# Kernel tuning notes

Hardware: AMD Instinct MI355X
Metric: run time of the kernel (lower is better)

The kernel has to match this reference:

```python
import jax, jax.numpy as jnp
import numpy as np

XY = 16   # xy_size
Z = 16    # z_size
S = XY * XY * Z   # num_states = 4096
V = 2048  # num_tokens


def _build_structure():
    # Static 3D-grid neighbor structure (replaces the per-state Python loop).
    h = np.arange(S)
    zc, rem = np.divmod(h, XY * XY)
    yc, xc = np.divmod(rem, XY)
    coords = np.stack([xc, yc, zc], 1)                       # [S,3] (x,y,z)
    offs = np.array([[0, 0, 0], [1, 0, 0], [-1, 0, 0], [0, 1, 0],
                     [0, -1, 0], [0, 0, 1], [0, 0, 2]])       # 7 fixed offsets
    nc = coords[:, None, :] + offs[None]                      # [S,7,3]
    valid = ((nc[..., 0] >= 0) & (nc[..., 0] < XY) &
             (nc[..., 1] >= 0) & (nc[..., 1] < XY) &
             (nc[..., 2] >= 0) & (nc[..., 2] < Z))
    dest = nc[..., 0] + XY * (nc[..., 1] + XY * nc[..., 2])   # flat neighbor idx
    # compact valid neighbors to the front, preserving offset order:
    # j-th valid neighbor consumes logit j (matches logits[h, :len(valid)])
    order = np.argsort(~valid, axis=1, kind='stable')
    tgt = np.take_along_axis(dest, order, axis=1)
    vmask = np.take_along_axis(valid, order, axis=1)
    tgt = np.where(vmask, tgt, S)  # invalid slots -> dummy column S
    return jnp.asarray(tgt), jnp.asarray(vmask)

TGT, VMASK = _build_structure()


def transition_log_p(trans_w):
    # masked log-softmax over the first k valid logits of each row
    logits = jnp.where(VMASK, trans_w, -1e30)
    logp = jax.nn.log_softmax(logits, axis=1)
    logp = jnp.where(VMASK, logp, -jnp.inf)
    T = jnp.full((S, S + 1), -jnp.inf, trans_w.dtype)
    T = T.at[jnp.arange(S)[:, None], TGT].set(logp)
    return T[:, :S]  # [S,S], row h = log p(transition targets of h)


def smoothed_emission(emis_w):
    em = jax.nn.log_softmax(emis_w, axis=-1).reshape(Z, XY, XY, V)
    lv, rv = em[:, :, :1], em[:, :, -1:]
    lh, rh = em[:, :1], em[:, -1:]
    c = jnp.zeros((Z, 1, 1, V), em.dtype)  # log(1)=0 pad, as in the original
    c2 = lambda *a: jnp.concatenate(a, axis=2)
    c1 = lambda *a: jnp.concatenate(a, axis=1)
    up = c1(c2(lv, em, rv), c2(c, rh, c), c2(c, rh, c))
    dn = c1(c2(c, lh, c), c2(c, lh, c), c2(lv, em, rv))
    lf = c1(c2(lh, c, c), c2(em, rv, rv), c2(rh, c, c))
    rt = c1(c2(c, c, lh), c2(lv, lv, em), c2(c, c, rh))
    cr = c1(c2(c, lh, c), c2(lv, em, rv), c2(c, rh, c))
    mean = jax.nn.logsumexp(jnp.stack((up, dn, lf, rt, cr)), axis=0) - jnp.log(5.0)
    return mean[:, 1:-1, 1:-1].reshape(S, V)


def _forward(stories, trans_w, emis_w, prior_w):
    priors = jax.nn.log_softmax(prior_w)                      # [S]
    em = smoothed_emission(emis_w)                            # [S,V]
    padded = jnp.concatenate([em, jnp.zeros((S, 1), em.dtype)], axis=1)  # [S,V+1]
    # per-(story, step) emission log-prob: sum over sentence tokens
    all_emis = padded.T[stories].sum(axis=2)                  # [B,L,S]
    all_emis = jnp.transpose(all_emis, (1, 0, 2))             # [L,B,S]
    T = transition_log_p(trans_w)                             # [S,S]
    amax = jnp.max(T, axis=1, keepdims=True)                  # [S,1], finite (self-loop)
    P = jnp.exp(T - amax)                                     # [S,S]
    score0 = all_emis[0] + priors                             # [B,S]

    def step(score, em_t):
        # new[b,a] = em_t[b,a] + logsumexp_h(T[a,h] + score[b,h])  (stable log-matmul)
        smax = jnp.max(score, axis=1, keepdims=True)          # [B,1]
        new = em_t + jnp.log(jnp.exp(score - smax) @ P.T) + smax + amax.T
        return new, new

    _, rest = jax.lax.scan(step, score0, all_emis[1:])
    return jnp.concatenate([score0[None], rest], axis=0)      # [L,B,S]


def setup_inputs() -> dict:
    key = jax.random.key(0)
    k1, k2, k3, k4 = jax.random.split(key, 4)
    B, L, W = 8, 32, 8
    return {
        "stories_tensor": jax.random.randint(k1, (B, L, W), 0, V + 1, dtype=jnp.int32),
        "story_length": L,
        "trans_w": jax.random.normal(k2, (S, 7), jnp.float32),
        "emis_w": jax.random.normal(k3, (S, V), jnp.float32),
        "prior_w": jax.random.normal(k4, (S,), jnp.float32),
    }


def reference(stories_tensor, story_length, trans_w, emis_w, prior_w):
    assert stories_tensor.shape[1] == story_length
    return _forward(stories_tensor, trans_w, emis_w, prior_w)
```

## Files before the change

kernel.cpp:

```cpp
#include <hip/hip_runtime.h>
#include <math.h>

#define XYD 16
#define ZD 16
#define SS 4096
#define VV 2048
#define BB 8
#define LL 32
#define WW 8
#define VC 32
#define SM_STRIDE 257

#define GUARD_L 16
#define GUARD_R 512
#define EBUF_N (GUARD_L + SS + GUARD_R)

#define BAR() asm volatile("s_waitcnt lgkmcnt(0)\n\ts_barrier" ::: "memory")

typedef unsigned short us8 __attribute__((ext_vector_type(8)));

__device__ __forceinline__ float b2f(unsigned short u) {
    union { unsigned int i; float f; } x; x.i = ((unsigned int)u) << 16; return x.f;
}
__device__ __forceinline__ unsigned short f2b(float f) {
    union { float f; unsigned int i; } x; x.f = f; return (unsigned short)(x.i >> 16);
}

__global__ void k_logZ(const float* __restrict__ emis_w, float* __restrict__ logZ) {
    int wave = threadIdx.x >> 6;
    int lane = threadIdx.x & 63;
    int row  = blockIdx.x * 4 + wave;
    const float* r = emis_w + (size_t)row * VV;
    float vals[32];
    float m = -INFINITY;
#pragma unroll
    for (int k = 0; k < 8; k++) {
        float4 f = ((const float4*)r)[k * 64 + lane];
        vals[k*4+0] = f.x; vals[k*4+1] = f.y; vals[k*4+2] = f.z; vals[k*4+3] = f.w;
    }
#pragma unroll
    for (int k = 0; k < 32; k++) m = fmaxf(m, vals[k]);
#pragma unroll
    for (int o = 32; o; o >>= 1) m = fmaxf(m, __shfl_xor(m, o));
    float sum = 0.f;
#pragma unroll
    for (int k = 0; k < 32; k++) sum += __expf(vals[k] - m);
#pragma unroll
    for (int o = 32; o; o >>= 1) sum += __shfl_xor(sum, o);
    if (lane == 0) logZ[row] = m + __logf(sum);
}

__global__ void k_smooth(const float* __restrict__ emis_w, const float* __restrict__ logZ,
                         unsigned short* __restrict__ smTb) {
    __shared__ float tileT[VC * SM_STRIDE];
    int z  = blockIdx.x;
    int v0 = blockIdx.y * VC;
    int tid = threadIdx.x;
    int rsub = tid >> 3;
    int c0   = (tid & 7) * 4;

#pragma unroll
    for (int it = 0; it < 8; it++) {
        int r  = it * 32 + rsub;
        int sg = z * 256 + r;
        float lz = logZ[sg];
        float4 w = *(const float4*)(emis_w + (size_t)sg * VV + v0 + c0);
        tileT[(c0+0)*SM_STRIDE + r] = __expf(w.x - lz);
        tileT[(c0+1)*SM_STRIDE + r] = __expf(w.y - lz);
        tileT[(c0+2)*SM_STRIDE + r] = __expf(w.z - lz);
        tileT[(c0+3)*SM_STRIDE + r] = __expf(w.w - lz);
    }
    __syncthreads();

    int x = tid & 15, y = tid >> 4;
    int sxp = (x < 15) ? tid + 1  : tid;
    int sxm = (x > 0)  ? tid - 1  : tid;
    int syp = (y < 15) ? tid + 16 : tid;
    int sym = (y > 0)  ? tid - 16 : tid;
    unsigned short* o = smTb + (size_t)v0 * SS + z * 256 + tid;
#pragma unroll
    for (int i = 0; i < VC; i++) {
        const float* tb = tileT + i * SM_STRIDE;
        float s = tb[tid] + tb[sxp] + tb[sxm] + tb[syp] + tb[sym];
        o[(size_t)i * SS] = f2b(__logf(s * 0.2f));
    }
}

__global__ void __launch_bounds__(512) k_emis(
    const int* __restrict__ stories, const unsigned short* __restrict__ smTb,
    float* __restrict__ all_emis) {
    int blk = blockIdx.x;
    int t = blk >> 3, b = blk & 7;
    int tid = threadIdx.x;
    int tok[WW];
#pragma unroll
    for (int w = 0; w < WW; w++) tok[w] = stories[(b * LL + t) * WW + w];
    int s0 = tid * 8;
    float acc[8] = {0.f,0.f,0.f,0.f,0.f,0.f,0.f,0.f};
#pragma unroll
    for (int w = 0; w < WW; w++) {
        if (tok[w] < VV) {
            us8 u = *(const us8*)(smTb + (size_t)tok[w] * SS + s0);
#pragma unroll
            for (int i = 0; i < 8; i++) acc[i] += b2f(u[i]);
        }
    }
    float* dst = all_emis + ((size_t)t * BB + b) * SS + s0;
    float4 lo = {acc[0], acc[1], acc[2], acc[3]};
    float4 hi = {acc[4], acc[5], acc[6], acc[7]};
    ((float4*)dst)[0] = lo;
    ((float4*)dst)[1] = hi;
}

__global__ void __launch_bounds__(1024) k_forward(
    const float* __restrict__ trans_w, const float* __restrict__ prior_w,
    const float* __restrict__ all_emis, float* __restrict__ out) {
    __shared__ __align__(16) unsigned short Ebuf[2][EBUF_N];
    __shared__ float red2[2];
    __shared__ float pr[16];
    int b = blockIdx.x;
    int tid = threadIdx.x;
    int lane = tid & 63, wid = tid >> 6;

    if (tid < GUARD_L) { Ebuf[0][tid] = 0; Ebuf[1][tid] = 0; }
    if (tid < GUARD_R) {
        Ebuf[0][GUARD_L + SS + tid] = 0;
        Ebuf[1][GUARD_L + SS + tid] = 0;
    }

    float pw[28], am[4];
    {
        float w7[28];
        const float4* t4 = (const float4*)(trans_w + (size_t)tid * 28);
#pragma unroll
        for (int k = 0; k < 7; k++) ((float4*)w7)[k] = t4[k];
#pragma unroll
        for (int i = 0; i < 4; i++) {
            int j = tid * 4 + i;
            int xx = j & 15, yy = (j >> 4) & 15, zz = j >> 8;
            bool val[7];
            val[0] = true;
            val[1] = (xx < 15); val[2] = (xx > 0);
            val[3] = (yy < 15); val[4] = (yy > 0);
            val[5] = (zz < 15); val[6] = (zz < 14);
            const float* rw = w7 + i * 7;
            float w[7]; int cnt = 0; float m = -INFINITY;
#pragma unroll
            for (int d = 0; d < 7; d++) { if (val[d]) { w[d] = rw[cnt++]; m = fmaxf(m, w[d]); } }
            float se = 0.f;
#pragma unroll
            for (int d = 0; d < 7; d++) if (val[d]) se += __expf(w[d] - m);
#pragma unroll
            for (int d = 0; d < 7; d++) pw[i*7+d] = val[d] ? __expf(w[d] - m) : 0.f;
            am[i] = -__logf(se);
        }
    }

    float4 pv = ((const float4*)prior_w)[tid];
    const float4* emp = (const float4*)(all_emis + (size_t)b * SS) + tid;
    float4 em = *emp;

    float lm = fmaxf(fmaxf(pv.x, pv.y), fmaxf(pv.z, pv.w));
#pragma unroll
    for (int o = 32; o; o >>= 1) lm = fmaxf(lm, __shfl_xor(lm, o));
    if (lane == 0) pr[wid] = lm;
    __syncthreads();
    float gm = pr[0];
#pragma unroll
    for (int w = 1; w < 16; w++) gm = fmaxf(gm, pr[w]);
    __syncthreads();
    float ls = __expf(pv.x - gm) + __expf(pv.y - gm) + __expf(pv.z - gm) + __expf(pv.w - gm);
#pragma unroll
    for (int o = 32; o; o >>= 1) ls += __shfl_xor(ls, o);
    if (lane == 0) pr[wid] = ls;
    __syncthreads();
    float gs = 0.f;
#pragma unroll
    for (int w = 0; w < 16; w++) gs += pr[w];
    float logZp = gm + __logf(gs);

    float v0 = em.x + pv.x - logZp;
    float v1 = em.y + pv.y - logZp;
    float v2 = em.z + pv.z - logZp;
    float v3 = em.w + pv.w - logZp;
    float4 ov_prev = {v0, v1, v2, v3};
    float4* outp = (float4*)(out + (size_t)b * SS) + tid;

    if (tid == 0) red2[0] = v0;
    __syncthreads();
    float g1 = red2[0];
    float XpPrev = g1;
    float E0 = __expf(v0 - XpPrev), E1 = __expf(v1 - XpPrev);
    float E2 = __expf(v2 - XpPrev), E3 = __expf(v3 - XpPrev);
    {
        ushort4 E;
        E.x = f2b(E0); E.y = f2b(E1); E.z = f2b(E2); E.w = f2b(E3);
        *(ushort4*)(&Ebuf[0][GUARD_L + 4 * tid]) = E;
    }

    emp += (BB * SS) / 4;
    float4 em_next = *emp;

    int cur = 0;
#pragma unroll 2
    for (int t = 1; t < LL; t++) {
        BAR();
        *outp = ov_prev;
        outp += (BB * SS) / 4;

        em = em_next;
        if (t < LL - 1) { emp += (BB * SS) / 4; em_next = *emp; }

        float cxw = __shfl_up(E3, 1);
        float bx  = __shfl_down(E0, 1);

        float g0 = red2[cur];
        float Xp = 2.f * g0 - g1;
        float dd = XpPrev - Xp;

        float s0 = em.x + am[0], s1 = em.y + am[1];
        float s2 = em.z + am[2], s3 = em.w + am[3];
        float K0 = __expf(s0 + dd), K1 = __expf(s1 + dd);
        float K2 = __expf(s2 + dd), K3 = __expf(s3 + dd);

        const unsigned short* Eb = Ebuf[cur] + GUARD_L + 4 * tid;
        ushort4 YpU = *(const ushort4*)(Eb + 16);
        ushort4 YmU = *(const ushort4*)(Eb - 16);
        ushort4 ZpU = *(const ushort4*)(Eb + 256);
        ushort4 ZqU = *(const ushort4*)(Eb + 512);

        float a0 = E0*pw[0]  + E1*pw[1]  + cxw*pw[2] + b2f(YpU.x)*pw[3]  + b2f(YmU.x)*pw[4]  + b2f(ZpU.x)*pw[5]  + b2f(ZqU.x)*pw[6];
        float a1 = E1*pw[7]  + E2*pw[8]  + E0*pw[9]  + b2f(YpU.y)*pw[10] + b2f(YmU.y)*pw[11] + b2f(ZpU.y)*pw[12] + b2f(ZqU.y)*pw[13];
        float a2 = E2*pw[14] + E3*pw[15] + E1*pw[16] + b2f(YpU.z)*pw[17] + b2f(YmU.z)*pw[18] + b2f(ZpU.z)*pw[19] + b2f(ZqU.z)*pw[20];
        float a3 = E3*pw[21] + bx*pw[22] + E2*pw[23] + b2f(YpU.w)*pw[24] + b2f(YmU.w)*pw[25] + b2f(ZpU.w)*pw[26] + b2f(ZqU.w)*pw[27];

        E0 = a0 * K0; E1 = a1 * K1; E2 = a2 * K2; E3 = a3 * K3;
        {
            ushort4 E;
            E.x = f2b(E0); E.y = f2b(E1); E.z = f2b(E2); E.w = f2b(E3);
            *(ushort4*)(&Ebuf[cur ^ 1][GUARD_L + 4 * tid]) = E;
        }

        v0 = s0 + __logf(a0) + XpPrev;
        v1 = s1 + __logf(a1) + XpPrev;
        v2 = s2 + __logf(a2) + XpPrev;
        v3 = s3 + __logf(a3) + XpPrev;
        ov_prev.x = v0; ov_prev.y = v1; ov_prev.z = v2; ov_prev.w = v3;

        if (tid == 0) red2[cur ^ 1] = v0;

        g1 = g0; XpPrev = Xp; cur ^= 1;
    }
    *outp = ov_prev;
}

extern "C" void kernel_launch(void* const* d_in, const int* in_sizes, int n_in,
                              void* d_out, int out_size, void* d_ws, size_t ws_size,
                              hipStream_t stream) {
    const int*   stories = (const int*)d_in[0];
    const float* trans_w = (const float*)d_in[2];
    const float* emis_w  = (const float*)d_in[3];
    const float* prior_w = (const float*)d_in[4];
    float* out = (float*)d_out;

    char* ws = (char*)d_ws;
    unsigned short* smTb = (unsigned short*)(ws);
    float* all_emis = (float*)(ws + (size_t)VV * SS * 2);
    float* logZ     = (float*)(ws + (size_t)VV * SS * 2 + (size_t)LL * BB * SS * 4);

    k_logZ<<<SS / 4, 256, 0, stream>>>(emis_w, logZ);
    k_smooth<<<dim3(ZD, VV / VC), 256, 0, stream>>>(emis_w, logZ, smTb);
    k_emis<<<LL * BB, 512, 0, stream>>>(stories, smTb, all_emis);
    k_forward<<<BB, 1024, 0, stream>>>(trans_w, prior_w, all_emis, out);
}
```

Measured before the change: 148.0 us.

## Replace per-step block barrier with per-wave flag sync over LDS ring buffer

Drops the whole-block barrier each timestep in the HMM forward scan. Each wave (one z-plane) now publishes its plane into a 4-deep LDS ring, sets a flag, and spin-waits only on the neighbouring planes it reads or overwrites. Each plane keeps its own scaling offset, taken from its own first element, and neighbour contributions are rescaled with exp(Xneighbor - Xcur), so waves can drift apart by a few steps. The cost is spin-polling with s_sleep, extra exp work for the z-neighbour scaling, and the risk of subtle ordering bugs in the flag protocol.

```diff
diff --git a/kernel.cpp b/kernel.cpp
--- a/kernel.cpp
+++ b/kernel.cpp
@@ -11,11 +11,11 @@
 #define VC 32
 #define SM_STRIDE 257
 
-#define GUARD_L 16
-#define GUARD_R 512
-#define EBUF_N (GUARD_L + SS + GUARD_R)
-
-#define BAR() asm volatile("s_waitcnt lgkmcnt(0)\n\ts_barrier" ::: "memory")
+#define RINGD 4
+#define ROWS 19
+
+#define LGKM0() asm volatile("s_waitcnt lgkmcnt(0)" ::: "memory")
+#define SFENCE() __builtin_amdgcn_sched_barrier(0)
 
 typedef unsigned short us8 __attribute__((ext_vector_type(8)));
 
@@ -115,17 +115,21 @@
 __global__ void __launch_bounds__(1024) k_forward(
     const float* __restrict__ trans_w, const float* __restrict__ prior_w,
     const float* __restrict__ all_emis, float* __restrict__ out) {
-    __shared__ __align__(16) unsigned short Ebuf[2][EBUF_N];
-    __shared__ float red2[2];
+    __shared__ __align__(16) unsigned short Ering[RINGD][ROWS][256];
+    __shared__ float Xring[RINGD][18];
+    __shared__ int flags[16];
     __shared__ float pr[16];
     int b = blockIdx.x;
     int tid = threadIdx.x;
-    int lane = tid & 63, wid = tid >> 6;
-
-    if (tid < GUARD_L) { Ebuf[0][tid] = 0; Ebuf[1][tid] = 0; }
-    if (tid < GUARD_R) {
-        Ebuf[0][GUARD_L + SS + tid] = 0;
-        Ebuf[1][GUARD_L + SS + tid] = 0;
+    int lane = tid & 63, z = tid >> 6;
+    volatile int* vf = flags;
+
+    {
+        unsigned int* E4 = (unsigned int*)&Ering[0][0][0];
+        const int n = RINGD * ROWS * 256 / 2;
+        for (int i = tid; i < n; i += 1024) E4[i] = 0u;
+        if (tid < RINGD * 18) (&Xring[0][0])[tid] = 0.f;
+        if (tid < 16) flags[tid] = -1;
     }
 
     float pw[28], am[4];
@@ -163,7 +167,7 @@
     float lm = fmaxf(fmaxf(pv.x, pv.y), fmaxf(pv.z, pv.w));
 #pragma unroll
     for (int o = 32; o; o >>= 1) lm = fmaxf(lm, __shfl_xor(lm, o));
-    if (lane == 0) pr[wid] = lm;
+    if (lane == 0) pr[z] = lm;
     __syncthreads();
     float gm = pr[0];
 #pragma unroll
@@ -172,86 +176,100 @@
     float ls = __expf(pv.x - gm) + __expf(pv.y - gm) + __expf(pv.z - gm) + __expf(pv.w - gm);
 #pragma unroll
     for (int o = 32; o; o >>= 1) ls += __shfl_xor(ls, o);
-    if (lane == 0) pr[wid] = ls;
+    if (lane == 0) pr[z] = ls;
     __syncthreads();
     float gs = 0.f;
 #pragma unroll
     for (int w = 0; w < 16; w++) gs += pr[w];
     float logZp = gm + __logf(gs);
+    __syncthreads();
 
     float v0 = em.x + pv.x - logZp;
     float v1 = em.y + pv.y - logZp;
     float v2 = em.z + pv.z - logZp;
     float v3 = em.w + pv.w - logZp;
-    float4 ov_prev = {v0, v1, v2, v3};
     float4* outp = (float4*)(out + (size_t)b * SS) + tid;
-
-    if (tid == 0) red2[0] = v0;
-    __syncthreads();
-    float g1 = red2[0];
-    float XpPrev = g1;
-    float E0 = __expf(v0 - XpPrev), E1 = __expf(v1 - XpPrev);
-    float E2 = __expf(v2 - XpPrev), E3 = __expf(v3 - XpPrev);
+    *outp = make_float4(v0, v1, v2, v3);
+    outp += (BB * SS) / 4;
+
+    float g = __uint_as_float(__builtin_amdgcn_readfirstlane(__float_as_uint(v0)));
+    float gp = g, gpp = g, Xcur = g;
+    float E0 = __expf(v0 - Xcur), E1 = __expf(v1 - Xcur);
+    float E2 = __expf(v2 - Xcur), E3 = __expf(v3 - Xcur);
     {
         ushort4 E;
         E.x = f2b(E0); E.y = f2b(E1); E.z = f2b(E2); E.w = f2b(E3);
-        *(ushort4*)(&Ebuf[0][GUARD_L + 4 * tid]) = E;
-    }
+        *(ushort4*)(&Ering[0][z + 1][4 * lane]) = E;
+        if (lane == 0) Xring[0][z] = Xcur;
+    }
+    LGKM0(); SFENCE();
+    if (lane == 0) vf[z] = 0;
 
     emp += (BB * SS) / 4;
     float4 em_next = *emp;
 
-    int cur = 0;
-#pragma unroll 2
+#pragma unroll 4
     for (int t = 1; t < LL; t++) {
-        BAR();
-        *outp = ov_prev;
-        outp += (BB * SS) / 4;
+        int sR = (t - 1) & (RINGD - 1);
+        int sW = t & (RINGD - 1);
 
         em = em_next;
         if (t < LL - 1) { emp += (BB * SS) / 4; em_next = *emp; }
 
-        float cxw = __shfl_up(E3, 1);
-        float bx  = __shfl_down(E0, 1);
-
-        float g0 = red2[cur];
-        float Xp = 2.f * g0 - g1;
-        float dd = XpPrev - Xp;
-
+        float Xnew = 2.f * gp - gpp;
+        float dd = Xcur - Xnew;
         float s0 = em.x + am[0], s1 = em.y + am[1];
         float s2 = em.z + am[2], s3 = em.w + am[3];
         float K0 = __expf(s0 + dd), K1 = __expf(s1 + dd);
         float K2 = __expf(s2 + dd), K3 = __expf(s3 + dd);
-
-        const unsigned short* Eb = Ebuf[cur] + GUARD_L + 4 * tid;
-        ushort4 YpU = *(const ushort4*)(Eb + 16);
-        ushort4 YmU = *(const ushort4*)(Eb - 16);
-        ushort4 ZpU = *(const ushort4*)(Eb + 256);
-        ushort4 ZqU = *(const ushort4*)(Eb + 512);
-
-        float a0 = E0*pw[0]  + E1*pw[1]  + cxw*pw[2] + b2f(YpU.x)*pw[3]  + b2f(YmU.x)*pw[4]  + b2f(ZpU.x)*pw[5]  + b2f(ZqU.x)*pw[6];
-        float a1 = E1*pw[7]  + E2*pw[8]  + E0*pw[9]  + b2f(YpU.y)*pw[10] + b2f(YmU.y)*pw[11] + b2f(ZpU.y)*pw[12] + b2f(ZqU.y)*pw[13];
-        float a2 = E2*pw[14] + E3*pw[15] + E1*pw[16] + b2f(YpU.z)*pw[17] + b2f(YmU.z)*pw[18] + b2f(ZpU.z)*pw[19] + b2f(ZqU.z)*pw[20];
-        float a3 = E3*pw[21] + bx*pw[22] + E2*pw[23] + b2f(YpU.w)*pw[24] + b2f(YmU.w)*pw[25] + b2f(ZpU.w)*pw[26] + b2f(ZqU.w)*pw[27];
+        float cxw = __shfl_up(E3, 1);
+        float bx  = __shfl_down(E0, 1);
+
+        if (z < 15) { while (vf[z + 1] < t - 1) __builtin_amdgcn_s_sleep(1); }
+        if (z < 14) { while (vf[z + 2] < t - 1) __builtin_amdgcn_s_sleep(1); }
+        if (z > 0)  { while (vf[z - 1] < t - 3) __builtin_amdgcn_s_sleep(1); }
+        if (z > 1)  { while (vf[z - 2] < t - 2) __builtin_amdgcn_s_sleep(1); }
+        SFENCE();
+
+        const unsigned short* pS = &Ering[sR][z + 1][4 * lane];
+        ushort4 YpU = *(const ushort4*)(pS + 16);
+        ushort4 YmU = *(const ushort4*)(pS - 16);
+        ushort4 ZpU = *(const ushort4*)(&Ering[sR][z + 2][4 * lane]);
+        ushort4 ZqU = *(const ushort4*)(&Ering[sR][z + 3][4 * lane]);
+        float XN1 = Xring[sR][z + 1];
+        float XN2 = Xring[sR][z + 2];
+        float f1 = (z < 15) ? __expf(XN1 - Xcur) : 0.f;
+        float f2 = (z < 14) ? __expf(XN2 - Xcur) : 0.f;
+
+        float a0 = E0*pw[0]  + E1*pw[1]  + cxw*pw[2] + b2f(YpU.x)*pw[3]  + b2f(YmU.x)*pw[4]
+                 + f1*(b2f(ZpU.x)*pw[5])  + f2*(b2f(ZqU.x)*pw[6]);
+        float a1 = E1*pw[7]  + E2*pw[8]  + E0*pw[9]  + b2f(YpU.y)*pw[10] + b2f(YmU.y)*pw[11]
+                 + f1*(b2f(ZpU.y)*pw[12]) + f2*(b2f(ZqU.y)*pw[13]);
+        float a2 = E2*pw[14] + E3*pw[15] + E1*pw[16] + b2f(YpU.z)*pw[17] + b2f(YmU.z)*pw[18]
+                 + f1*(b2f(ZpU.z)*pw[19]) + f2*(b2f(ZqU.z)*pw[20]);
+        float a3 = E3*pw[21] + bx*pw[22] + E2*pw[23] + b2f(YpU.w)*pw[24] + b2f(YmU.w)*pw[25]
+                 + f1*(b2f(ZpU.w)*pw[26]) + f2*(b2f(ZqU.w)*pw[27]);
 
         E0 = a0 * K0; E1 = a1 * K1; E2 = a2 * K2; E3 = a3 * K3;
         {
             ushort4 E;
             E.x = f2b(E0); E.y = f2b(E1); E.z = f2b(E2); E.w = f2b(E3);
-            *(ushort4*)(&Ebuf[cur ^ 1][GUARD_L + 4 * tid]) = E;
+            *(ushort4*)(&Ering[sW][z + 1][4 * lane]) = E;
+            if (lane == 0) Xring[sW][z] = Xnew;
         }
-
-        v0 = s0 + __logf(a0) + XpPrev;
-        v1 = s1 + __logf(a1) + XpPrev;
-        v2 = s2 + __logf(a2) + XpPrev;
-        v3 = s3 + __logf(a3) + XpPrev;
-        ov_prev.x = v0; ov_prev.y = v1; ov_prev.z = v2; ov_prev.w = v3;
-
-        if (tid == 0) red2[cur ^ 1] = v0;
-
-        g1 = g0; XpPrev = Xp; cur ^= 1;
-    }
-    *outp = ov_prev;
+        LGKM0(); SFENCE();
+        if (lane == 0) vf[z] = t;
+
+        v0 = s0 + __logf(a0) + Xcur;
+        v1 = s1 + __logf(a1) + Xcur;
+        v2 = s2 + __logf(a2) + Xcur;
+        v3 = s3 + __logf(a3) + Xcur;
+        *outp = make_float4(v0, v1, v2, v3);
+        outp += (BB * SS) / 4;
+
+        g = __uint_as_float(__builtin_amdgcn_readfirstlane(__float_as_uint(v0)));
+        gpp = gp; gp = g; Xcur = Xnew;
+    }
 }
 
 extern "C" void kernel_launch(void* const* d_in, const int* in_sizes, int n_in,
```

New measurement: 176.3 us. 1.19x slower.

## Fuse emission gather into forward kernel with one-step prefetch

Applied to the files above, without the earlier changes.

Removes the separate k_emis kernel and its all_emis intermediate buffer. The forward kernel now keeps the story tokens in shared memory and gathers the smoothed bf16 emission rows itself, prefetching the rows for step t+1 while step t runs. This saves a kernel launch and the write and read of the emission tensor. In exchange, the serial 8-block forward loop now performs 8 scattered gathers per step and holds more registers, which may add latency to the critical path.

```diff
diff --git a/kernel.cpp b/kernel.cpp
--- a/kernel.cpp
+++ b/kernel.cpp
@@ -86,38 +86,14 @@
     }
 }
 
-__global__ void __launch_bounds__(512) k_emis(
-    const int* __restrict__ stories, const unsigned short* __restrict__ smTb,
-    float* __restrict__ all_emis) {
-    int blk = blockIdx.x;
-    int t = blk >> 3, b = blk & 7;
-    int tid = threadIdx.x;
-    int tok[WW];
-#pragma unroll
-    for (int w = 0; w < WW; w++) tok[w] = stories[(b * LL + t) * WW + w];
-    int s0 = tid * 8;
-    float acc[8] = {0.f,0.f,0.f,0.f,0.f,0.f,0.f,0.f};
-#pragma unroll
-    for (int w = 0; w < WW; w++) {
-        if (tok[w] < VV) {
-            us8 u = *(const us8*)(smTb + (size_t)tok[w] * SS + s0);
-#pragma unroll
-            for (int i = 0; i < 8; i++) acc[i] += b2f(u[i]);
-        }
-    }
-    float* dst = all_emis + ((size_t)t * BB + b) * SS + s0;
-    float4 lo = {acc[0], acc[1], acc[2], acc[3]};
-    float4 hi = {acc[4], acc[5], acc[6], acc[7]};
-    ((float4*)dst)[0] = lo;
-    ((float4*)dst)[1] = hi;
-}
-
 __global__ void __launch_bounds__(1024) k_forward(
-    const float* __restrict__ trans_w, const float* __restrict__ prior_w,
-    const float* __restrict__ all_emis, float* __restrict__ out) {
+    const int* __restrict__ stories, const float* __restrict__ trans_w,
+    const float* __restrict__ prior_w, const unsigned short* __restrict__ smTb,
+    float* __restrict__ out) {
     __shared__ __align__(16) unsigned short Ebuf[2][EBUF_N];
     __shared__ float red2[2];
     __shared__ float pr[16];
+    __shared__ int stl[LL * WW];
     int b = blockIdx.x;
     int tid = threadIdx.x;
     int lane = tid & 63, wid = tid >> 6;
@@ -127,6 +103,7 @@
         Ebuf[0][GUARD_L + SS + tid] = 0;
         Ebuf[1][GUARD_L + SS + tid] = 0;
     }
+    if (tid < LL * WW) stl[tid] = stories[b * (LL * WW) + tid];
 
     float pw[28], am[4];
     {
@@ -157,8 +134,6 @@
     }
 
     float4 pv = ((const float4*)prior_w)[tid];
-    const float4* emp = (const float4*)(all_emis + (size_t)b * SS) + tid;
-    float4 em = *emp;
 
     float lm = fmaxf(fmaxf(pv.x, pv.y), fmaxf(pv.z, pv.w));
 #pragma unroll
@@ -179,10 +154,25 @@
     for (int w = 0; w < 16; w++) gs += pr[w];
     float logZp = gm + __logf(gs);
 
-    float v0 = em.x + pv.x - logZp;
-    float v1 = em.y + pv.y - logZp;
-    float v2 = em.z + pv.z - logZp;
-    float v3 = em.w + pv.w - logZp;
+    const size_t gidx = 4 * (size_t)tid;
+    ushort4 gb[WW];
+#pragma unroll
+    for (int w = 0; w < WW; w++) {
+        int tk = stl[w];
+        if (tk < VV) gb[w] = *(const ushort4*)(smTb + (size_t)tk * SS + gidx);
+        else         gb[w] = make_ushort4(0, 0, 0, 0);
+    }
+    float emx = 0.f, emy = 0.f, emz = 0.f, emw = 0.f;
+#pragma unroll
+    for (int w = 0; w < WW; w++) {
+        emx += b2f(gb[w].x); emy += b2f(gb[w].y);
+        emz += b2f(gb[w].z); emw += b2f(gb[w].w);
+    }
+
+    float v0 = emx + pv.x - logZp;
+    float v1 = emy + pv.y - logZp;
+    float v2 = emz + pv.z - logZp;
+    float v3 = emw + pv.w - logZp;
     float4 ov_prev = {v0, v1, v2, v3};
     float4* outp = (float4*)(out + (size_t)b * SS) + tid;
 
@@ -198,28 +188,44 @@
         *(ushort4*)(&Ebuf[0][GUARD_L + 4 * tid]) = E;
     }
 
-    emp += (BB * SS) / 4;
-    float4 em_next = *emp;
+#pragma unroll
+    for (int w = 0; w < WW; w++) {
+        int tk = stl[WW + w];
+        if (tk < VV) gb[w] = *(const ushort4*)(smTb + (size_t)tk * SS + gidx);
+        else         gb[w] = make_ushort4(0, 0, 0, 0);
+    }
 
     int cur = 0;
 #pragma unroll 2
     for (int t = 1; t < LL; t++) {
+        emx = 0.f; emy = 0.f; emz = 0.f; emw = 0.f;
+#pragma unroll
+        for (int w = 0; w < WW; w++) {
+            emx += b2f(gb[w].x); emy += b2f(gb[w].y);
+            emz += b2f(gb[w].z); emw += b2f(gb[w].w);
+        }
+        if (t < LL - 1) {
+#pragma unroll
+            for (int w = 0; w < WW; w++) {
+                int tk = stl[(t + 1) * WW + w];
+                if (tk < VV) gb[w] = *(const ushort4*)(smTb + (size_t)tk * SS + gidx);
+                else         gb[w] = make_ushort4(0, 0, 0, 0);
+            }
+        }
+
+        float cxw = __shfl_up(E3, 1);
+        float bx  = __shfl_down(E0, 1);
+
         BAR();
         *outp = ov_prev;
         outp += (BB * SS) / 4;
 
-        em = em_next;
-        if (t < LL - 1) { emp += (BB * SS) / 4; em_next = *emp; }
-
-        float cxw = __shfl_up(E3, 1);
-        float bx  = __shfl_down(E0, 1);
-
         float g0 = red2[cur];
         float Xp = 2.f * g0 - g1;
         float dd = XpPrev - Xp;
 
-        float s0 = em.x + am[0], s1 = em.y + am[1];
-        float s2 = em.z + am[2], s3 = em.w + am[3];
+        float s0 = emx + am[0], s1 = emy + am[1];
+        float s2 = emz + am[2], s3 = emw + am[3];
         float K0 = __expf(s0 + dd), K1 = __expf(s1 + dd);
         float K2 = __expf(s2 + dd), K3 = __expf(s3 + dd);
 
@@ -265,11 +271,9 @@
 
     char* ws = (char*)d_ws;
     unsigned short* smTb = (unsigned short*)(ws);
-    float* all_emis = (float*)(ws + (size_t)VV * SS * 2);
-    float* logZ     = (float*)(ws + (size_t)VV * SS * 2 + (size_t)LL * BB * SS * 4);
+    float* logZ = (float*)(ws + (size_t)VV * SS * 2);
 
     k_logZ<<<SS / 4, 256, 0, stream>>>(emis_w, logZ);
     k_smooth<<<dim3(ZD, VV / VC), 256, 0, stream>>>(emis_w, logZ, smTb);
-    k_emis<<<LL * BB, 512, 0, stream>>>(stories, smTb, all_emis);
-    k_forward<<<BB, 1024, 0, stream>>>(trans_w, prior_w, all_emis, out);
-}
+    k_forward<<<BB, 1024, 0, stream>>>(stories, trans_w, prior_w, smTb, out);
+}
```

Result: slower. 179.6 us (+21.3%).

## Precompute bf16 emission probabilities and vectorize smoothing stencil stores

Applied to the files above, without the earlier changes.

The first kernel now also writes normalized emission probabilities as bf16 into workspace, so the smoothing kernel reads half-width data and needs no exp. That avoids a second full fp32 read of emis_w. The smoothing stencil is restructured so each thread computes two adjacent states, using float2 shared-memory loads and packed 32-bit stores, with the LDS stride changed to 258 for alignment. Probabilities are rounded to bf16 before the stencil sum, which adds a little error, and the new path only runs if the workspace holds at least 36 MB, otherwise the old path is used.

```diff
diff --git a/kernel.cpp b/kernel.cpp
--- a/kernel.cpp
+++ b/kernel.cpp
@@ -9,7 +9,7 @@
 #define LL 32
 #define WW 8
 #define VC 32
-#define SM_STRIDE 257
+#define SM_STRIDE 258
 
 #define GUARD_L 16
 #define GUARD_R 512
@@ -24,6 +24,40 @@
 }
 __device__ __forceinline__ unsigned short f2b(float f) {
     union { float f; unsigned int i; } x; x.f = f; return (unsigned short)(x.i >> 16);
+}
+
+__global__ void k_prob(const float* __restrict__ emis_w, unsigned short* __restrict__ qb) {
+    int wave = threadIdx.x >> 6;
+    int lane = threadIdx.x & 63;
+    int row  = blockIdx.x * 4 + wave;
+    const float* r = emis_w + (size_t)row * VV;
+    float vals[32];
+    float m = -INFINITY;
+#pragma unroll
+    for (int k = 0; k < 8; k++) {
+        float4 f = ((const float4*)r)[k * 64 + lane];
+        vals[k*4+0] = f.x; vals[k*4+1] = f.y; vals[k*4+2] = f.z; vals[k*4+3] = f.w;
+    }
+#pragma unroll
+    for (int k = 0; k < 32; k++) m = fmaxf(m, vals[k]);
+#pragma unroll
+    for (int o = 32; o; o >>= 1) m = fmaxf(m, __shfl_xor(m, o));
+    float sum = 0.f;
+#pragma unroll
+    for (int k = 0; k < 32; k++) sum += __expf(vals[k] - m);
+#pragma unroll
+    for (int o = 32; o; o >>= 1) sum += __shfl_xor(sum, o);
+    float lz = m + __logf(sum);
+    unsigned short* qr = qb + (size_t)row * VV;
+#pragma unroll
+    for (int k = 0; k < 8; k++) {
+        ushort4 q;
+        q.x = f2b(__expf(vals[k*4+0] - lz));
+        q.y = f2b(__expf(vals[k*4+1] - lz));
+        q.z = f2b(__expf(vals[k*4+2] - lz));
+        q.w = f2b(__expf(vals[k*4+3] - lz));
+        ((ushort4*)qr)[k * 64 + lane] = q;
+    }
 }
 
 __global__ void k_logZ(const float* __restrict__ emis_w, float* __restrict__ logZ) {
@@ -50,40 +84,76 @@
     if (lane == 0) logZ[row] = m + __logf(sum);
 }
 
-__global__ void k_smooth(const float* __restrict__ emis_w, const float* __restrict__ logZ,
-                         unsigned short* __restrict__ smTb) {
+__device__ __forceinline__ void smooth_phase2(const float* __restrict__ tileT,
+                                              unsigned short* __restrict__ smTb,
+                                              int z, int v0, int tid) {
+    int u = tid & 127, vh = tid >> 7;
+    int s0 = 2 * u;
+    int e = s0 & 15, y0 = s0 >> 4;
+    int ixm = (e > 0)   ? s0 - 1  : s0;
+    int ixp = (e < 14)  ? s0 + 2  : s0 + 1;
+    int iym = (y0 > 0)  ? s0 - 16 : s0;
+    int iyp = (y0 < 15) ? s0 + 16 : s0;
+    unsigned int* o = (unsigned int*)(smTb + (size_t)(v0 + vh * 16) * SS + z * 256 + s0);
+#pragma unroll
+    for (int i = 0; i < 16; i++) {
+        const float* tb = tileT + (vh * 16 + i) * SM_STRIDE;
+        float2 c01 = *(const float2*)(tb + s0);
+        float xmv = tb[ixm];
+        float xpv = tb[ixp];
+        float2 ymv = *(const float2*)(tb + iym);
+        float2 ypv = *(const float2*)(tb + iyp);
+        float sA = c01.x + c01.y + xmv + ymv.x + ypv.x;
+        float sB = c01.x + c01.y + xpv + ymv.y + ypv.y;
+        unsigned int qa = (unsigned int)f2b(__logf(sA * 0.2f));
+        unsigned int qc = (unsigned int)f2b(__logf(sB * 0.2f));
+        o[(size_t)i * (SS / 2)] = qa | (qc << 16);
+    }
+}
+
+__global__ void k_smooth_q(const unsigned short* __restrict__ qb,
+                           unsigned short* __restrict__ smTb) {
     __shared__ float tileT[VC * SM_STRIDE];
     int z  = blockIdx.x;
     int v0 = blockIdx.y * VC;
     int tid = threadIdx.x;
     int rsub = tid >> 3;
     int c0   = (tid & 7) * 4;
-
 #pragma unroll
     for (int it = 0; it < 8; it++) {
         int r  = it * 32 + rsub;
         int sg = z * 256 + r;
-        float lz = logZ[sg];
+        ushort4 u4 = *(const ushort4*)(qb + (size_t)sg * VV + v0 + c0);
+        tileT[(c0+0)*SM_STRIDE + r] = b2f(u4.x);
+        tileT[(c0+1)*SM_STRIDE + r] = b2f(u4.y);
+        tileT[(c0+2)*SM_STRIDE + r] = b2f(u4.z);
+        tileT[(c0+3)*SM_STRIDE + r] = b2f(u4.w);
+    }
+    __syncthreads();
+    smooth_phase2(tileT, smTb, z, v0, tid);
+}
+
+__global__ void k_smooth_f(const float* __restrict__ emis_w, const float* __restrict__ logZ,
+                           unsigned short* __restrict__ smTb) {
+    __shared__ float tileT[VC * SM_STRIDE];
+    int z  = blockIdx.x;
+    int v0 = blockIdx.y * VC;
+    int tid = threadIdx.x;
+    int rsub = tid >> 3;
+    int c0   = (tid & 7) * 4;
+#pragma unroll
+    for (int it = 0; it < 8; it++) {
+        int r  = it * 32 + rsub;
+        int sg = z * 256 + r;
+        float lzv = logZ[sg];
         float4 w = *(const float4*)(emis_w + (size_t)sg * VV + v0 + c0);
-        tileT[(c0+0)*SM_STRIDE + r] = __expf(w.x - lz);
-        tileT[(c0+1)*SM_STRIDE + r] = __expf(w.y - lz);
-        tileT[(c0+2)*SM_STRIDE + r] = __expf(w.z - lz);
-        tileT[(c0+3)*SM_STRIDE + r] = __expf(w.w - lz);
-    }
-    __syncthreads();
-
-    int x = tid & 15, y = tid >> 4;
-    int sxp = (x < 15) ? tid + 1  : tid;
-    int sxm = (x > 0)  ? tid - 1  : tid;
-    int syp = (y < 15) ? tid + 16 : tid;
-    int sym = (y > 0)  ? tid - 16 : tid;
-    unsigned short* o = smTb + (size_t)v0 * SS + z * 256 + tid;
-#pragma unroll
-    for (int i = 0; i < VC; i++) {
-        const float* tb = tileT + i * SM_STRIDE;
-        float s = tb[tid] + tb[sxp] + tb[sxm] + tb[syp] + tb[sym];
-        o[(size_t)i * SS] = f2b(__logf(s * 0.2f));
-    }
+        tileT[(c0+0)*SM_STRIDE + r] = __expf(w.x - lzv);
+        tileT[(c0+1)*SM_STRIDE + r] = __expf(w.y - lzv);
+        tileT[(c0+2)*SM_STRIDE + r] = __expf(w.z - lzv);
+        tileT[(c0+3)*SM_STRIDE + r] = __expf(w.w - lzv);
+    }
+    __syncthreads();
+    smooth_phase2(tileT, smTb, z, v0, tid);
 }
 
 __global__ void __launch_bounds__(512) k_emis(
@@ -266,10 +336,16 @@
     char* ws = (char*)d_ws;
     unsigned short* smTb = (unsigned short*)(ws);
     float* all_emis = (float*)(ws + (size_t)VV * SS * 2);
-    float* logZ     = (float*)(ws + (size_t)VV * SS * 2 + (size_t)LL * BB * SS * 4);
-
-    k_logZ<<<SS / 4, 256, 0, stream>>>(emis_w, logZ);
-    k_smooth<<<dim3(ZD, VV / VC), 256, 0, stream>>>(emis_w, logZ, smTb);
+
+    if (ws_size >= (size_t)36 * 1024 * 1024) {
+        unsigned short* qb = (unsigned short*)(ws + (size_t)20 * 1024 * 1024);
+        k_prob<<<SS / 4, 256, 0, stream>>>(emis_w, qb);
+        k_smooth_q<<<dim3(ZD, VV / VC), 256, 0, stream>>>(qb, smTb);
+    } else {
+        float* logZ = (float*)(ws + (size_t)VV * SS * 2 + (size_t)LL * BB * SS * 4);
+        k_logZ<<<SS / 4, 256, 0, stream>>>(emis_w, logZ);
+        k_smooth_f<<<dim3(ZD, VV / VC), 256, 0, stream>>>(emis_w, logZ, smTb);
+    }
     k_emis<<<LL * BB, 512, 0, stream>>>(stories, smTb, all_emis);
     k_forward<<<BB, 1024, 0, stream>>>(trans_w, prior_w, all_emis, out);
 }
```

After: 148.1 us. No clear change (+0.0%).
